# Kernel tuning notes

Measured on AMD Instinct MI355X. Metric: run time of the kernel, lower is better.

## Reference

```python
import jax, jax.numpy as jnp
import numpy as np

L, B, V, E, H = 128, 64, 10000, 512, 512


def setup_inputs() -> dict:
    key = jax.random.key(0)
    ks = jax.random.split(key, 12)
    s = 0.05
    seq = jax.random.randint(ks[0], (L, B), 0, V, dtype=jnp.int32)
    seq_length = jnp.full((B,), L, dtype=jnp.int32)  # equal lengths -> pack/pad identity
    return {
        "seq": seq,
        "seq_length": seq_length,
        "emb": jax.random.normal(ks[1], (V, E), jnp.float32) * 0.01,  # matches init.normal std=0.01
        "W_ih_f": jax.random.normal(ks[2], (3 * H, E), jnp.float32) * s,
        "W_hh_f": jax.random.normal(ks[3], (3 * H, H), jnp.float32) * s,
        "b_ih_f": jax.random.normal(ks[4], (3 * H,), jnp.float32) * s,
        "b_hh_f": jax.random.normal(ks[5], (3 * H,), jnp.float32) * s,
        "W_ih_b": jax.random.normal(ks[6], (3 * H, E), jnp.float32) * s,
        "W_hh_b": jax.random.normal(ks[7], (3 * H, H), jnp.float32) * s,
        "b_ih_b": jax.random.normal(ks[8], (3 * H,), jnp.float32) * s,
        "b_hh_b": jax.random.normal(ks[9], (3 * H,), jnp.float32) * s,
        "dec_W": jax.random.normal(ks[10], (V, 2 * H), jnp.float32) * s,
        "dec_b": jax.random.normal(ks[11], (V,), jnp.float32) * s,
    }


def _gru(x_emb, W_ih, W_hh, b_ih, b_hh, reverse):
    # x_emb: [L, B, E]; PyTorch GRU cell equations.
    gx = jnp.einsum('lbe,ge->lbg', x_emb, W_ih) + b_ih  # [L, B, 3H]
    h0 = jnp.zeros((x_emb.shape[1], W_hh.shape[1]), x_emb.dtype)

    def step(h, gx_t):
        gh = h @ W_hh.T + b_hh
        r = jax.nn.sigmoid(gx_t[:, :H] + gh[:, :H])
        z = jax.nn.sigmoid(gx_t[:, H:2 * H] + gh[:, H:2 * H])
        n = jnp.tanh(gx_t[:, 2 * H:] + r * gh[:, 2 * H:])
        h_new = (1.0 - z) * n + z * h
        return h_new, h_new

    _, ys = jax.lax.scan(step, h0, gx, reverse=reverse)
    return ys  # [L, B, H], aligned with input positions


def reference(seq, seq_length, emb, W_ih_f, W_hh_f, b_ih_f, b_hh_f,
              W_ih_b, W_hh_b, b_ih_b, b_hh_b, dec_W, dec_b):
    x = emb[seq]  # [L, B, E]; dropout=0 (eval) -> identity
    out_f = _gru(x, W_ih_f, W_hh_f, b_ih_f, b_hh_f, reverse=False)  # [L, B, H]
    out_b = _gru(x, W_ih_b, W_hh_b, b_ih_b, b_hh_b, reverse=True)   # [L, B, H]
    # EditType.REPLACE: fwd state before the edited token, bwd state after it
    out = jnp.concatenate([out_f[0:L - 2], out_b[2:L]], axis=2)  # [L-2, B, 2H]
    logits = jnp.einsum('lbh,vh->lbv', out, dec_W) + dec_b       # [L-2, B, V]
    return jax.nn.log_softmax(logits, axis=-1)
```

## Files before the change

### kernel.cpp

```cpp
#include <hip/hip_runtime.h>
#include <hip/hip_bf16.h>
#include <stdint.h>

#define LL 128
#define BB 64
#define VV 10000
#define EE 512
#define HH 512
#define G3 1536
#define MROWS 8192
#define DM 8064
#define D2H 1024
#define NPAD 10112
#define FP 16

typedef __bf16 bf16x8 __attribute__((ext_vector_type(8)));
typedef float f32x4 __attribute__((ext_vector_type(4)));
typedef int i32x4 __attribute__((ext_vector_type(4)));
typedef unsigned int u32x4 __attribute__((ext_vector_type(4)));
typedef unsigned short u16;

static __device__ __forceinline__ float bf2f(u16 u) {
  unsigned int x = ((unsigned int)u) << 16;
  return __builtin_bit_cast(float, x);
}
static __device__ __forceinline__ u16 f2bf(float f) {
  unsigned int x = __builtin_bit_cast(unsigned int, f);
  unsigned int r = x + 0x7FFFu + ((x >> 16) & 1u);
  return (u16)(r >> 16);
}
static __device__ __forceinline__ signed char q8(float v) {
  float r = fminf(fmaxf(rintf(v), -127.f), 127.f);
  return (signed char)(int)r;
}

static __device__ __forceinline__ void cstore16(void* p, u32x4 v) {
  asm volatile("global_store_dwordx4 %0, %1, off sc0 sc1" :: "v"(p), "v"(v) : "memory");
}
static __device__ __forceinline__ void flagstore4(void* p, int v) {
  asm volatile("global_store_dword %0, %1, off sc0 sc1" :: "v"(p), "v"(v) : "memory");
}
static __device__ __forceinline__ int flagload4(const void* p) {
  int v;
  asm volatile("global_load_dword %0, %1, off sc0 sc1\n\ts_waitcnt vmcnt(0)"
               : "=v"(v) : "v"(p) : "memory");
  return v;
}
static __device__ __forceinline__ void gload_lds16(const void* g, void* s) {
  __builtin_amdgcn_global_load_lds(
      (const __attribute__((address_space(1))) unsigned int*)g,
      (__attribute__((address_space(3))) unsigned int*)s, 16, 0, 0);
}

__global__ void k_cast(const float4* __restrict__ src, ushort4* __restrict__ dst, int n4) {
  int i = blockIdx.x * blockDim.x + threadIdx.x;
  if (i < n4) {
    float4 v = src[i];
    ushort4 o;
    o.x = f2bf(v.x); o.y = f2bf(v.y); o.z = f2bf(v.z); o.w = f2bf(v.w);
    dst[i] = o;
  }
}

__global__ __launch_bounds__(256) void k_quant_w(const float* __restrict__ W,
                                                 signed char* __restrict__ Q,
                                                 float* __restrict__ wscale) {
  const int v = blockIdx.x;
  const int tid = threadIdx.x;
  const int l = tid & 63, w = tid >> 6;
  float4 x = *(const float4*)(W + (long)v * 1024 + tid * 4);
  float m = fmaxf(fmaxf(fabsf(x.x), fabsf(x.y)), fmaxf(fabsf(x.z), fabsf(x.w)));
#pragma unroll
  for (int off = 32; off; off >>= 1) m = fmaxf(m, __shfl_xor(m, off));
  __shared__ float red[4];
  __shared__ float s_inv;
  if (l == 0) red[w] = m;
  __syncthreads();
  if (tid == 0) {
    float mm = fmaxf(fmaxf(red[0], red[1]), fmaxf(red[2], red[3]));
    mm = fmaxf(mm, 1e-12f);
    s_inv = 127.f / mm;
    wscale[v] = mm / (127.f * 127.f);
  }
  __syncthreads();
  float inv = s_inv;
  char4 o;
  o.x = q8(x.x * inv); o.y = q8(x.y * inv); o.z = q8(x.z * inv); o.w = q8(x.w * inv);
  *(char4*)(Q + (long)v * 1024 + tid * 4) = o;
}

__global__ void k_quant_a(const u16* __restrict__ src, signed char* __restrict__ Q, int n4) {
  int i = blockIdx.x * 256 + threadIdx.x;
  if (i < n4) {
    ushort4 u = ((const ushort4*)src)[i];
    char4 o;
    o.x = q8(bf2f(u.x) * 127.f); o.y = q8(bf2f(u.y) * 127.f);
    o.z = q8(bf2f(u.z) * 127.f); o.w = q8(bf2f(u.w) * 127.f);
    ((char4*)Q)[i] = o;
  }
}

__global__ void k_embed(const int* __restrict__ seq, const float* __restrict__ emb,
                        u16* __restrict__ x) {
  int rb = blockIdx.x;
  int v = seq[rb];
  const float4* s = (const float4*)(emb + (long)v * EE);
  ushort4* d = (ushort4*)(x + (long)rb * EE);
  int t = threadIdx.x;
  float4 val = s[t];
  ushort4 o;
  o.x = f2bf(val.x); o.y = f2bf(val.y); o.z = f2bf(val.z); o.w = f2bf(val.w);
  d[t] = o;
}

template<int OUTF32>
__global__ __launch_bounds__(256) void k_gemm(
    const u16* __restrict__ A, const u16* __restrict__ B,
    const float* __restrict__ bias, void* __restrict__ C,
    int lda, int ldb, int ldc, int K, int ncols)
{
  __shared__ char smem[32768];
  const int tid = threadIdx.x;
  const int l = tid & 63;
  const int w = tid >> 6;
  const int wr = w >> 1, wc = w & 1;
  const long tM = (long)blockIdx.x * 128;
  const long tN = (long)blockIdx.y * 128;

  f32x4 acc[4][4];
#pragma unroll
  for (int m = 0; m < 4; m++)
#pragma unroll
    for (int n = 0; n < 4; n++) acc[m][n] = {0.f, 0.f, 0.f, 0.f};

  const int nk = K >> 6;
  for (int kt = 0; kt < nk; ++kt) {
    const int k0 = kt << 6;
#pragma unroll
    for (int i = 0; i < 4; i++) {
      int cchunk = w * 4 + i;
      int c = cchunk * 64 + l;
      int row = c >> 3, k8 = c & 7;
      gload_lds16(A + (tM + row) * lda + k0 + k8 * 8, smem + cchunk * 1024);
      gload_lds16(B + (tN + row) * ldb + k0 + k8 * 8, smem + 16384 + cchunk * 1024);
    }
    __syncthreads();
#pragma unroll
    for (int kk = 0; kk < 2; kk++) {
      const int kb = kk * 64 + ((l >> 4) * 16);
      bf16x8 af[4], bfr[4];
#pragma unroll
      for (int m = 0; m < 4; m++) {
        int ra = wr * 64 + m * 16 + (l & 15);
        af[m] = *(const bf16x8*)(smem + ra * 128 + kb);
      }
#pragma unroll
      for (int n = 0; n < 4; n++) {
        int rb2 = wc * 64 + n * 16 + (l & 15);
        bfr[n] = *(const bf16x8*)(smem + 16384 + rb2 * 128 + kb);
      }
#pragma unroll
      for (int m = 0; m < 4; m++)
#pragma unroll
        for (int n = 0; n < 4; n++)
          acc[m][n] = __builtin_amdgcn_mfma_f32_16x16x32_bf16(af[m], bfr[n], acc[m][n], 0, 0, 0);
    }
    __syncthreads();
  }
#pragma unroll
  for (int n = 0; n < 4; n++) {
    long col = tN + wc * 64 + n * 16 + (l & 15);
    float bv = (col < ncols) ? bias[col] : 0.f;
    if (col < ncols) {
#pragma unroll
      for (int m = 0; m < 4; m++) {
        long row = tM + wr * 64 + m * 16 + ((l >> 4) * 4);
#pragma unroll
        for (int r = 0; r < 4; r++) {
          float v = acc[m][n][r] + bv;
          if (OUTF32) ((float*)C)[(row + r) * ldc + col] = v;
          else        ((u16*)C)[(row + r) * ldc + col] = f2bf(v);
        }
      }
    }
  }
}

__global__ __launch_bounds__(256) void k_gemm_i8(
    const signed char* __restrict__ A,
    const signed char* __restrict__ B,
    const float* __restrict__ wscale,
    const float* __restrict__ bias,
    float* __restrict__ C)
{
  __shared__ char smem[32768];
  const int tid = threadIdx.x;
  const int l = tid & 63;
  const int w = tid >> 6;
  const int wr = w >> 1, wc = w & 1;
  const long tM = (long)blockIdx.x * 128;
  const long tN = (long)blockIdx.y * 128;

  i32x4 acc[4][4];
#pragma unroll
  for (int m = 0; m < 4; m++)
#pragma unroll
    for (int n = 0; n < 4; n++) acc[m][n] = {0, 0, 0, 0};

  for (int kt = 0; kt < 8; ++kt) {
    const int k0 = kt << 7;
#pragma unroll
    for (int i = 0; i < 4; i++) {
      int j = w * 4 + i;
      int row = j * 8 + (l >> 3);
      int k16 = l & 7;
      gload_lds16(A + (tM + row) * 1024 + k0 + k16 * 16, smem + j * 1024);
      gload_lds16(B + (tN + row) * 1024 + k0 + k16 * 16, smem + 16384 + j * 1024);
    }
    __syncthreads();
#pragma unroll
    for (int ks = 0; ks < 2; ks++) {
      const int kb = ks * 64 + ((l >> 4) * 16);
      i32x4 af[4], bfr[4];
#pragma unroll
      for (int m = 0; m < 4; m++) {
        int ra = wr * 64 + m * 16 + (l & 15);
        af[m] = *(const i32x4*)(smem + ra * 128 + kb);
      }
#pragma unroll
      for (int n = 0; n < 4; n++) {
        int rb2 = wc * 64 + n * 16 + (l & 15);
        bfr[n] = *(const i32x4*)(smem + 16384 + rb2 * 128 + kb);
      }
#pragma unroll
      for (int m = 0; m < 4; m++)
#pragma unroll
        for (int n = 0; n < 4; n++)
          acc[m][n] = __builtin_amdgcn_mfma_i32_16x16x64_i8(af[m], bfr[n], acc[m][n], 0, 0, 0);
    }
    __syncthreads();
  }
#pragma unroll
  for (int n = 0; n < 4; n++) {
    long col = tN + wc * 64 + n * 16 + (l & 15);
    if (col < VV) {
      float sc = wscale[col];
      float bv = bias[col];
#pragma unroll
      for (int m = 0; m < 4; m++) {
        long row = tM + wr * 64 + m * 16 + ((l >> 4) * 4);
#pragma unroll
        for (int r = 0; r < 4; r++)
          C[(row + r) * VV + col] = (float)acc[m][n][r] * sc + bv;
      }
    }
  }
}

__global__ __launch_bounds__(256) void k_gru(
    const u16* __restrict__ Whh_all,
    const float* __restrict__ bhh_f, const float* __restrict__ bhh_b,
    const u16* __restrict__ gx_all,
    u16* __restrict__ hsteps,
    u16* __restrict__ cat,
    int* __restrict__ bar16)
{
  const int blk = blockIdx.x;
  const int dir = blockIdx.y;
  const int tid = threadIdx.x;
  const int l = tid & 63, w = tid >> 6;
  const u16* Whh = Whh_all + (long)dir * G3 * HH;
  const float* bhh = dir ? bhh_b : bhh_f;
  const u16* gx = gx_all + (long)dir * MROWS * G3;

  __shared__ char Wl[96 * 1024];
  __shared__ __align__(16) u16 hstage[BB][32];

  for (int c = tid; c < 6144; c += 256) {
    int lr = c >> 6;
    int k8 = c & 63;
    int gr = (lr >> 5) * HH + blk * 32 + (lr & 31);
    uint4 v = *(const uint4*)(Whh + (long)gr * HH + k8 * 8);
    *(uint4*)(Wl + lr * 1024 + ((k8 * 16) ^ ((lr & 7) << 4))) = v;
  }
  float bh[6];
#pragma unroll
  for (int n = 0; n < 6; n++) {
    int c = n * 16 + (l & 15);
    bh[n] = bhh[(c >> 5) * HH + blk * 32 + (c & 31)];
  }
  float hreg[4][2] = {};
  __syncthreads();

  const int lrow = w * 16 + ((l >> 4) * 4);
  const int srow = tid >> 2, schunk = tid & 3;

  for (int t = 0; t < LL; ++t) {
    const int lpos = dir ? (LL - 1 - t) : t;
    const u16* hsrc = hsteps + ((size_t)t * 2 + dir) * BB * HH;

    bf16x8 af[16];
    {
      const u16* hrow = hsrc + (w * 16 + (l & 15)) * HH + ((l >> 4) * 8);
#pragma unroll
      for (int kc = 0; kc < 16; kc++) af[kc] = *(const bf16x8*)(hrow + kc * 32);
    }
    u16 gxv[3][4][2];
#pragma unroll
    for (int r = 0; r < 4; r++) {
      const u16* gxr = gx + ((long)lpos * BB + (lrow + r)) * G3 + blk * 32;
#pragma unroll
      for (int g = 0; g < 3; g++)
#pragma unroll
        for (int p = 0; p < 2; p++)
          gxv[g][r][p] = gxr[g * HH + p * 16 + (l & 15)];
    }

    f32x4 acc[6];
#pragma unroll
    for (int n = 0; n < 6; n++) acc[n] = {0.f, 0.f, 0.f, 0.f};
#pragma unroll
    for (int kc = 0; kc < 16; kc++) {
      const int kb = kc * 64 + ((l >> 4) * 16);
#pragma unroll
      for (int n = 0; n < 6; n++) {
        int lr = n * 16 + (l & 15);
        bf16x8 bfr = *(const bf16x8*)(Wl + lr * 1024 + (kb ^ ((l & 7) << 4)));
        acc[n] = __builtin_amdgcn_mfma_f32_16x16x32_bf16(af[kc], bfr, acc[n], 0, 0, 0);
      }
    }

#pragma unroll
    for (int r = 0; r < 4; r++) {
#pragma unroll
      for (int p = 0; p < 2; p++) {
        float ghr = acc[0 + p][r] + bh[0 + p];
        float ghz = acc[2 + p][r] + bh[2 + p];
        float ghn = acc[4 + p][r] + bh[4 + p];
        float xr = bf2f(gxv[0][r][p]);
        float xz = bf2f(gxv[1][r][p]);
        float xn = bf2f(gxv[2][r][p]);
        float ar = fminf(fmaxf(xr + ghr, -30.f), 30.f);
        float az = fminf(fmaxf(xz + ghz, -30.f), 30.f);
        float rg = 1.f / (1.f + __expf(-ar));
        float zg = 1.f / (1.f + __expf(-az));
        float an = fminf(fmaxf(xn + rg * ghn, -30.f), 30.f);
        float e2 = __expf(-2.f * an);
        float ng = (1.f - e2) / (1.f + e2);
        float hn = (1.f - zg) * ng + zg * hreg[r][p];
        hreg[r][p] = hn;
        hstage[lrow + r][p * 16 + (l & 15)] = f2bf(hn);
      }
    }
    __syncthreads();

    u32x4 hv = *(const u32x4*)&hstage[srow][schunk * 8];
    if (t < LL - 1) {
      u16* hdst = hsteps + ((size_t)(t + 1) * 2 + dir) * BB * HH;
      cstore16(hdst + srow * HH + blk * 32 + schunk * 8, hv);
      asm volatile("s_waitcnt vmcnt(0)" ::: "memory");
      __syncthreads();
      if (tid == 0)
        flagstore4(&bar16[((dir * LL + t) * 16 + blk) * FP], 1);
      const int* flg = bar16 + (dir * LL + t) * 16 * FP;
      for (;;) {
        int v = 1;
        if (l < 16) v = flagload4(&flg[l * FP]);
        if (__all(v != 0)) break;
      }
      __builtin_amdgcn_sched_barrier(0);
    }
    if (dir == 0) {
      if (lpos < LL - 2)
        *(u32x4*)(cat + ((long)lpos * BB + srow) * D2H + blk * 32 + schunk * 8) = hv;
    } else {
      if (lpos >= 2)
        *(u32x4*)(cat + ((long)(lpos - 2) * BB + srow) * D2H + HH + blk * 32 + schunk * 8) = hv;
    }
  }
}

__global__ __launch_bounds__(256) void k_lsm(float* __restrict__ out) {
  const long row = blockIdx.x;
  float* p = out + row * VV;
  const int tid = threadIdx.x;
  const int l = tid & 63, w = tid >> 6;
  __shared__ float red[8];

  float4 v[10];
  float m = -1e30f;
#pragma unroll
  for (int j = 0; j < 10; j++) {
    int idx = j * 256 + tid;
    if (idx < 2500) {
      v[j] = *(float4*)(p + idx * 4);
      m = fmaxf(m, fmaxf(fmaxf(v[j].x, v[j].y), fmaxf(v[j].z, v[j].w)));
    }
  }
#pragma unroll
  for (int off = 32; off; off >>= 1) m = fmaxf(m, __shfl_xor(m, off));
  if (l == 0) red[w] = m;
  __syncthreads();
  m = fmaxf(fmaxf(red[0], red[1]), fmaxf(red[2], red[3]));

  float s = 0.f;
#pragma unroll
  for (int j = 0; j < 10; j++) {
    int idx = j * 256 + tid;
    if (idx < 2500) {
      s += __expf(v[j].x - m) + __expf(v[j].y - m) + __expf(v[j].z - m) + __expf(v[j].w - m);
    }
  }
#pragma unroll
  for (int off = 32; off; off >>= 1) s += __shfl_xor(s, off);
  if (l == 0) red[4 + w] = s;
  __syncthreads();
  s = red[4] + red[5] + red[6] + red[7];
  float lse = m + logf(s);

#pragma unroll
  for (int j = 0; j < 10; j++) {
    int idx = j * 256 + tid;
    if (idx < 2500) {
      float4 o;
      o.x = v[j].x - lse; o.y = v[j].y - lse; o.z = v[j].z - lse; o.w = v[j].w - lse;
      *(float4*)(p + idx * 4) = o;
    }
  }
}

extern "C" void kernel_launch(void* const* d_in, const int* in_sizes, int n_in,
                              void* d_out, int out_size, void* d_ws, size_t ws_size,
                              hipStream_t stream) {
  const int*   seq  = (const int*)d_in[0];
  const float* emb  = (const float*)d_in[2];
  const float* Wihf = (const float*)d_in[3];
  const float* Whhf = (const float*)d_in[4];
  const float* bihf = (const float*)d_in[5];
  const float* bhhf = (const float*)d_in[6];
  const float* Wihb = (const float*)d_in[7];
  const float* Whhb = (const float*)d_in[8];
  const float* bihb = (const float*)d_in[9];
  const float* bhhb = (const float*)d_in[10];
  const float* decW = (const float*)d_in[11];
  const float* decb = (const float*)d_in[12];

  char* ws = (char*)d_ws;
  size_t off = 0;
  u16* Whh_bf = (u16*)(ws + off); off += (size_t)2 * G3 * HH * 2;
  u16* Wih_bf = (u16*)(ws + off); off += (size_t)2 * G3 * EE * 2;
  signed char* decWq = (signed char*)(ws + off); off += (size_t)NPAD * 1024;
  float* wscale = (float*)(ws + off); off += (size_t)NPAD * 4;
  u16* xb = (u16*)(ws + off); off += (size_t)MROWS * EE * 2;
  u16* gxb = (u16*)(ws + off); off += (size_t)2 * MROWS * G3 * 2;
  u16* cat = (u16*)(ws + off); off += (size_t)DM * D2H * 2;
  signed char* catq = (signed char*)(ws + off); off += (size_t)DM * D2H;
  u16* hsteps = (u16*)(ws + off); off += (size_t)(LL + 1) * 2 * BB * HH * 2;
  int* bar16 = (int*)(ws + off); off += (size_t)2 * LL * 16 * FP * 4;

  (void)hipMemsetAsync(hsteps, 0, (size_t)2 * BB * HH * 2, stream);
  (void)hipMemsetAsync(bar16, 0, (size_t)2 * LL * 16 * FP * 4, stream);

  const int n4w = G3 * HH / 4;
  k_cast<<<(n4w + 255) / 256, 256, 0, stream>>>((const float4*)Whhf, (ushort4*)(Whh_bf), n4w);
  k_cast<<<(n4w + 255) / 256, 256, 0, stream>>>((const float4*)Whhb, (ushort4*)(Whh_bf + G3 * HH), n4w);
  k_cast<<<(n4w + 255) / 256, 256, 0, stream>>>((const float4*)Wihf, (ushort4*)(Wih_bf), n4w);
  k_cast<<<(n4w + 255) / 256, 256, 0, stream>>>((const float4*)Wihb, (ushort4*)(Wih_bf + G3 * EE), n4w);
  k_quant_w<<<VV, 256, 0, stream>>>(decW, decWq, wscale);
  k_embed<<<MROWS, 128, 0, stream>>>(seq, emb, xb);

  k_gemm<0><<<dim3(64, 12), 256, 0, stream>>>(xb, Wih_bf, bihf, gxb, EE, EE, G3, EE, G3);
  k_gemm<0><<<dim3(64, 12), 256, 0, stream>>>(xb, Wih_bf + G3 * EE, bihb, gxb + (size_t)MROWS * G3, EE, EE, G3, EE, G3);

  k_gru<<<dim3(16, 2), 256, 0, stream>>>(Whh_bf, bhhf, bhhb, gxb, hsteps, cat, bar16);

  k_quant_a<<<(DM * D2H / 4 + 255) / 256, 256, 0, stream>>>(cat, catq, DM * D2H / 4);
  k_gemm_i8<<<dim3(63, 79), 256, 0, stream>>>(catq, decWq, wscale, decb, (float*)d_out);

  k_lsm<<<DM, 256, 0, stream>>>((float*)d_out);
}
```

Baseline: 1.212 ms.

## Fuse activation int8 quantization into GRU and prefetch next-step gate inputs

```diff
diff --git a/kernel.cpp b/kernel.cpp
--- a/kernel.cpp
+++ b/kernel.cpp
@@ -19,6 +19,7 @@
 typedef int i32x4 __attribute__((ext_vector_type(4)));
 typedef unsigned int u32x4 __attribute__((ext_vector_type(4)));
 typedef unsigned short u16;
+typedef unsigned long long u64;
 
 static __device__ __forceinline__ float bf2f(u16 u) {
   unsigned int x = ((unsigned int)u) << 16;
@@ -87,17 +88,6 @@
   char4 o;
   o.x = q8(x.x * inv); o.y = q8(x.y * inv); o.z = q8(x.z * inv); o.w = q8(x.w * inv);
   *(char4*)(Q + (long)v * 1024 + tid * 4) = o;
-}
-
-__global__ void k_quant_a(const u16* __restrict__ src, signed char* __restrict__ Q, int n4) {
-  int i = blockIdx.x * 256 + threadIdx.x;
-  if (i < n4) {
-    ushort4 u = ((const ushort4*)src)[i];
-    char4 o;
-    o.x = q8(bf2f(u.x) * 127.f); o.y = q8(bf2f(u.y) * 127.f);
-    o.z = q8(bf2f(u.z) * 127.f); o.w = q8(bf2f(u.w) * 127.f);
-    ((char4*)Q)[i] = o;
-  }
 }
 
 __global__ void k_embed(const int* __restrict__ seq, const float* __restrict__ emb,
@@ -262,7 +252,7 @@
     const float* __restrict__ bhh_f, const float* __restrict__ bhh_b,
     const u16* __restrict__ gx_all,
     u16* __restrict__ hsteps,
-    u16* __restrict__ cat,
+    signed char* __restrict__ catq,
     int* __restrict__ bar16)
 {
   const int blk = blockIdx.x;
@@ -275,6 +265,7 @@
 
   __shared__ char Wl[96 * 1024];
   __shared__ __align__(16) u16 hstage[BB][32];
+  __shared__ __align__(8) signed char hstageq[BB][32];
 
   for (int c = tid; c < 6144; c += 256) {
     int lr = c >> 6;
@@ -295,25 +286,37 @@
   const int lrow = w * 16 + ((l >> 4) * 4);
   const int srow = tid >> 2, schunk = tid & 3;
 
+  u16 gxn[3][4][2];
+  {
+    const int lpos0 = dir ? (LL - 1) : 0;
+#pragma unroll
+    for (int r = 0; r < 4; r++) {
+      const u16* gxr = gx + ((long)lpos0 * BB + (lrow + r)) * G3 + blk * 32;
+#pragma unroll
+      for (int g = 0; g < 3; g++)
+#pragma unroll
+        for (int p = 0; p < 2; p++)
+          gxn[g][r][p] = gxr[g * HH + p * 16 + (l & 15)];
+    }
+  }
+
   for (int t = 0; t < LL; ++t) {
     const int lpos = dir ? (LL - 1 - t) : t;
     const u16* hsrc = hsteps + ((size_t)t * 2 + dir) * BB * HH;
 
+    u16 gxv[3][4][2];
+#pragma unroll
+    for (int g = 0; g < 3; g++)
+#pragma unroll
+      for (int r = 0; r < 4; r++)
+#pragma unroll
+        for (int p = 0; p < 2; p++) gxv[g][r][p] = gxn[g][r][p];
+
     bf16x8 af[16];
     {
       const u16* hrow = hsrc + (w * 16 + (l & 15)) * HH + ((l >> 4) * 8);
 #pragma unroll
       for (int kc = 0; kc < 16; kc++) af[kc] = *(const bf16x8*)(hrow + kc * 32);
-    }
-    u16 gxv[3][4][2];
-#pragma unroll
-    for (int r = 0; r < 4; r++) {
-      const u16* gxr = gx + ((long)lpos * BB + (lrow + r)) * G3 + blk * 32;
-#pragma unroll
-      for (int g = 0; g < 3; g++)
-#pragma unroll
-        for (int p = 0; p < 2; p++)
-          gxv[g][r][p] = gxr[g * HH + p * 16 + (l & 15)];
     }
 
     f32x4 acc[6];
@@ -350,11 +353,13 @@
         float hn = (1.f - zg) * ng + zg * hreg[r][p];
         hreg[r][p] = hn;
         hstage[lrow + r][p * 16 + (l & 15)] = f2bf(hn);
+        hstageq[lrow + r][p * 16 + (l & 15)] = q8(hn * 127.f);
       }
     }
     __syncthreads();
 
     u32x4 hv = *(const u32x4*)&hstage[srow][schunk * 8];
+    u64 hq = *(const u64*)&hstageq[srow][schunk * 8];
     if (t < LL - 1) {
       u16* hdst = hsteps + ((size_t)(t + 1) * 2 + dir) * BB * HH;
       cstore16(hdst + srow * HH + blk * 32 + schunk * 8, hv);
@@ -362,6 +367,25 @@
       __syncthreads();
       if (tid == 0)
         flagstore4(&bar16[((dir * LL + t) * 16 + blk) * FP], 1);
+      {
+        const int lposn = dir ? (LL - 2 - t) : (t + 1);
+#pragma unroll
+        for (int r = 0; r < 4; r++) {
+          const u16* gxr = gx + ((long)lposn * BB + (lrow + r)) * G3 + blk * 32;
+#pragma unroll
+          for (int g = 0; g < 3; g++)
+#pragma unroll
+            for (int p = 0; p < 2; p++)
+              gxn[g][r][p] = gxr[g * HH + p * 16 + (l & 15)];
+        }
+      }
+      if (dir == 0) {
+        if (lpos < LL - 2)
+          *(u64*)(catq + ((long)lpos * BB + srow) * D2H + blk * 32 + schunk * 8) = hq;
+      } else {
+        if (lpos >= 2)
+          *(u64*)(catq + ((long)(lpos - 2) * BB + srow) * D2H + HH + blk * 32 + schunk * 8) = hq;
+      }
       const int* flg = bar16 + (dir * LL + t) * 16 * FP;
       for (;;) {
         int v = 1;
@@ -369,13 +393,14 @@
         if (__all(v != 0)) break;
       }
       __builtin_amdgcn_sched_barrier(0);
-    }
-    if (dir == 0) {
-      if (lpos < LL - 2)
-        *(u32x4*)(cat + ((long)lpos * BB + srow) * D2H + blk * 32 + schunk * 8) = hv;
     } else {
-      if (lpos >= 2)
-        *(u32x4*)(cat + ((long)(lpos - 2) * BB + srow) * D2H + HH + blk * 32 + schunk * 8) = hv;
+      if (dir == 0) {
+        if (lpos < LL - 2)
+          *(u64*)(catq + ((long)lpos * BB + srow) * D2H + blk * 32 + schunk * 8) = hq;
+      } else {
+        if (lpos >= 2)
+          *(u64*)(catq + ((long)(lpos - 2) * BB + srow) * D2H + HH + blk * 32 + schunk * 8) = hq;
+      }
     }
   }
 }
@@ -453,7 +478,6 @@
   float* wscale = (float*)(ws + off); off += (size_t)NPAD * 4;
   u16* xb = (u16*)(ws + off); off += (size_t)MROWS * EE * 2;
   u16* gxb = (u16*)(ws + off); off += (size_t)2 * MROWS * G3 * 2;
-  u16* cat = (u16*)(ws + off); off += (size_t)DM * D2H * 2;
   signed char* catq = (signed char*)(ws + off); off += (size_t)DM * D2H;
   u16* hsteps = (u16*)(ws + off); off += (size_t)(LL + 1) * 2 * BB * HH * 2;
   int* bar16 = (int*)(ws + off); off += (size_t)2 * LL * 16 * FP * 4;
@@ -472,9 +496,8 @@
   k_gemm<0><<<dim3(64, 12), 256, 0, stream>>>(xb, Wih_bf, bihf, gxb, EE, EE, G3, EE, G3);
   k_gemm<0><<<dim3(64, 12), 256, 0, stream>>>(xb, Wih_bf + G3 * EE, bihb, gxb + (size_t)MROWS * G3, EE, EE, G3, EE, G3);
 
-  k_gru<<<dim3(16, 2), 256, 0, stream>>>(Whh_bf, bhhf, bhhb, gxb, hsteps, cat, bar16);
-
-  k_quant_a<<<(DM * D2H / 4 + 255) / 256, 256, 0, stream>>>(cat, catq, DM * D2H / 4);
+  k_gru<<<dim3(16, 2), 256, 0, stream>>>(Whh_bf, bhhf, bhhb, gxb, hsteps, catq, bar16);
+
   k_gemm_i8<<<dim3(63, 79), 256, 0, stream>>>(catq, decWq, wscale, decb, (float*)d_out);
 
   k_lsm<<<DM, 256, 0, stream>>>((float*)d_out);
```

Result: faster. 1.183 ms (-2.4%).
